# Kernel tuning notes

Measured on AMD Instinct MI355X. Metric: run time of the kernel, lower is better.

## Reference

```python
import jax, jax.numpy as jnp
import numpy as np

# Config (from TheoreticalConfig, scaled to production size)
B = 4096          # batch_size
S = 128           # seq_len (max_seq_len)
DIM_Q = 512
DIM_Z = 64
DIM_U = 512
HID_V = 512       # assumed net_V hidden width
T_OFF = 20        # T_offline
T_ON = 10         # T_online
DT = 0.1
STIFF = 0.1       # stiffness
CSTIFF = 0.1      # contact_stiffness
MIN_DIM = min(DIM_U, DIM_Q)  # == DIM_Q here


def setup_inputs() -> dict:
    key = jax.random.key(0)
    ks = jax.random.split(key, 10)
    f32 = jnp.float32
    return {
        "u_seq": jax.random.normal(ks[0], (B, S, DIM_U), f32),
        "q0_off": jax.random.normal(ks[1], (B, DIM_Q), f32) * 0.1,
        "p0_off": jax.random.normal(ks[2], (B, DIM_Q), f32) * 0.1,
        "q0_on": jax.random.normal(ks[3], (B, DIM_Q), f32) * 0.1,
        "p0_on": jax.random.normal(ks[4], (B, DIM_Q), f32) * 0.1,
        "z": jax.random.normal(ks[5], (1, DIM_Z), f32) * 0.1,
        "W1": jax.random.normal(ks[6], (DIM_Q + DIM_Z, HID_V), f32) / np.sqrt(DIM_Q + DIM_Z).astype(np.float32),
        "b1": jnp.zeros((HID_V,), f32),
        "W2": jax.random.normal(ks[7], (HID_V, 1), f32) / np.sqrt(HID_V).astype(np.float32),
        "b2": jnp.zeros((1,), f32),
    }


def _net_V(qz, W1, b1, W2, b2):
    # small MLP potential: [B, dim_q+dim_z] -> [B, 1]
    return jnp.tanh(qz @ W1 + b1) @ W2 + b2


def _compute_H(q, p, s, z, W1, b1, W2, b2):
    # H^c = K + V_quad + V_net + Phi, all [B, 1]
    K = 0.5 * jnp.sum(p * p, axis=-1, keepdims=True)
    V_quad = 0.5 * STIFF * jnp.sum(q * q, axis=-1, keepdims=True)
    V_net = _net_V(jnp.concatenate([q, z], axis=-1), W1, b1, W2, b2)
    Phi = 0.5 * CSTIFF * s * s
    return K + V_quad + V_net + Phi


def reference(u_seq, q0_off, p0_off, q0_on, p0_on, z, W1, b1, W2, b2):
    zb = jnp.broadcast_to(z, (B, DIM_Z))
    s = jnp.zeros((B, 1), u_seq.dtype)

    # ---- evolve_offline: symplectic-ish leapfrog with friction, T_OFF-1 steps ----
    F0_off = _compute_H(q0_off, p0_off, s, zb, W1, b1, W2, b2)

    def off_step(carry, _):
        q, p = carry
        q_new = q + DT * p                     # q += dt * grad_p (grad_p = p)
        p_new = (p - DT * (STIFF * q)) * 0.99  # p -= dt * grad_q (grad_q = stiff*q_old), then damping
        return (q_new, p_new), None

    (qf, pf), _ = jax.lax.scan(off_step, (q0_off, p0_off), None, length=T_OFF - 1)
    Ff_off = _compute_H(qf, pf, s, zb, W1, b1, W2, b2)
    offline_F = jnp.concatenate([F0_off, Ff_off], axis=1)  # [B, 2]

    # ---- evolve_online: port-coupled integration for min(S, T_ON) steps ----
    F0_on = _compute_H(q0_on, p0_on, s, zb, W1, b1, W2, b2)
    steps = min(S, T_ON)

    def on_step(carry, u_t):
        q, p = carry
        # p_new[:, :MIN_DIM] = p - dt*stiff*q + dt*0.1*u_t ; MIN_DIM == DIM_Q so full update
        p_new = (p - DT * (STIFF * q) + DT * (0.1 * u_t)) * 0.99
        q_new = q + DT * p_new
        return (q_new, p_new), None

    u_scan = jnp.transpose(u_seq[:, :steps, :MIN_DIM], (1, 0, 2))  # [steps, B, dim_q]
    (qf2, pf2), _ = jax.lax.scan(on_step, (q0_on, p0_on), u_scan)
    Ff_on = _compute_H(qf2, pf2, s, zb, W1, b1, W2, b2)
    online_F = jnp.concatenate([F0_on, Ff_on], axis=1)  # [B, 2]

    q_trajectory = qf2[:, None, :]  # [B, 1, dim_q]
    return offline_F, online_F, q_trajectory
```

## Files before the change

kernel.cpp:

```cpp
#include <hip/hip_runtime.h>
#include <hip/hip_bf16.h>

#define BB 4096
#define SS 128
#define DIMQ 512
#define DIMZ 64
#define DIMU 512
#define HIDV 512

typedef __attribute__((ext_vector_type(8))) short sh8;
typedef __attribute__((ext_vector_type(4))) float f32x4;
typedef __attribute__((ext_vector_type(4))) unsigned short us4;

__device__ inline unsigned short f2bf(float f) {
    unsigned u = __float_as_uint(f);
    return (unsigned short)((u + 0x7fffu + ((u >> 16) & 1u)) >> 16);
}

__global__ __launch_bounds__(256) void k_prep(const float* __restrict__ W1,
        const float* __restrict__ z, const float* __restrict__ b1,
        unsigned short* __restrict__ W1qT, float* __restrict__ cvec) {
    __shared__ float tile[32][33];
    int bx = blockIdx.x & 15, by = blockIdx.x >> 4;
    int k0 = by * 32, n0 = bx * 32;
    int tx = threadIdx.x & 31, tg = threadIdx.x >> 5;
    #pragma unroll
    for (int rr = 0; rr < 4; rr++) {
        int ty = tg * 4 + rr;
        tile[ty][tx] = W1[(size_t)(k0 + ty) * HIDV + n0 + tx];
    }
    __syncthreads();
    #pragma unroll
    for (int rr = 0; rr < 4; rr++) {
        int ty = tg * 4 + rr;
        W1qT[(size_t)(n0 + ty) * DIMQ + k0 + tx] = f2bf(tile[tx][ty]);
    }
    if (blockIdx.x < 2) {
        int h = blockIdx.x * 256 + threadIdx.x;
        float acc = b1[h];
        #pragma unroll 8
        for (int k = 0; k < DIMZ; k++) acc += z[k] * W1[(size_t)(DIMQ + k) * HIDV + h];
        cvec[h] = acc;
    }
}

__global__ __launch_bounds__(128) void k_states(
        const float* __restrict__ u, const float* __restrict__ q0off,
        const float* __restrict__ p0off, const float* __restrict__ q0on,
        const float* __restrict__ p0on, const float* __restrict__ b2,
        unsigned short* __restrict__ Qall, float* __restrict__ out,
        float* __restrict__ qtraj,
        float R00, float R01, float R10, float R11) {
    int b = blockIdx.x, t = threadIdx.x;
    int j = t * 4;
    size_t idx = (size_t)b * DIMQ + j;
    float q[4], p[4], qo[4], po[4];
    *(float4*)q  = *(const float4*)(q0off + idx);
    *(float4*)p  = *(const float4*)(p0off + idx);
    *(float4*)qo = *(const float4*)(q0on + idx);
    *(float4*)po = *(const float4*)(p0on + idx);

    float sums[8] = {0, 0, 0, 0, 0, 0, 0, 0};
    us4 w0, w1, w2, w3;
    float q2[4], p2[4];
    #pragma unroll
    for (int c = 0; c < 4; c++) {
        float qq = q[c], pp = p[c];
        sums[0] += qq * qq;
        sums[1] += pp * pp;
        float qf = R00 * qq + R01 * pp;
        float pf = R10 * qq + R11 * pp;
        sums[2] += qf * qf;
        sums[3] += pf * pf;
        w0[c] = f2bf(qq);
        w1[c] = f2bf(qf);
        q2[c] = qo[c]; p2[c] = po[c];
        sums[4] += q2[c] * q2[c];
        sums[5] += p2[c] * p2[c];
        w2[c] = f2bf(q2[c]);
    }
    *(us4*)(Qall + idx) = w0;
    *(us4*)(Qall + (size_t)(BB + b) * DIMQ + j) = w1;
    *(us4*)(Qall + (size_t)(2 * BB + b) * DIMQ + j) = w2;

    const float* ub = u + (size_t)b * SS * DIMU + j;
    #pragma unroll
    for (int st = 0; st < 10; st++) {
        float uv[4];
        *(float4*)uv = *(const float4*)(ub + (size_t)st * DIMU);
        #pragma unroll
        for (int c = 0; c < 4; c++) {
            p2[c] = (p2[c] - 0.1f * (0.1f * q2[c]) + 0.1f * (0.1f * uv[c])) * 0.99f;
            q2[c] = q2[c] + 0.1f * p2[c];
        }
    }
    #pragma unroll
    for (int c = 0; c < 4; c++) {
        sums[6] += q2[c] * q2[c];
        sums[7] += p2[c] * p2[c];
        w3[c] = f2bf(q2[c]);
    }
    *(us4*)(Qall + (size_t)(3 * BB + b) * DIMQ + j) = w3;
    *(float4*)(qtraj + idx) = *(float4*)q2;

    __shared__ float red[2][8];
    int lane = t & 63, w = t >> 6;
    #pragma unroll
    for (int k = 0; k < 8; k++) {
        float v = sums[k];
        #pragma unroll
        for (int m = 1; m < 64; m <<= 1) v += __shfl_xor(v, m, 64);
        if (lane == 0) red[w][k] = v;
    }
    __syncthreads();
    if (t < 4) {
        int e = t;
        float sq = red[0][2 * e] + red[1][2 * e];
        float sp = red[0][2 * e + 1] + red[1][2 * e + 1];
        float F = 0.5f * sp + 0.05f * sq + b2[0];
        size_t o = (size_t)b * 2 + (e & 1) + (size_t)(e >> 1) * 2 * BB;
        out[o] = F;
    }
}

__global__ __launch_bounds__(256) void k_gemm(
        const unsigned short* __restrict__ Qall, const unsigned short* __restrict__ W1qT,
        const float* __restrict__ cvec, const float* __restrict__ W2,
        float* __restrict__ out) {
    __shared__ __attribute__((aligned(16))) char lds[65536];
    const int t = threadIdx.x;
    const int lane = t & 63;
    const int w = t >> 6;
    const int wr = w >> 1, wc = w & 1;
    const int rowBase = blockIdx.x * 128;
    const int colBase = blockIdx.y * 128;

    f32x4 acc[4][4] = {};

    auto STAGE = [&](int kt, int buf) {
        char* ldsA = lds + buf * 32768;
        char* ldsB = ldsA + 16384;
        #pragma unroll
        for (int i = 0; i < 4; i++) {
            unsigned chunk = i * 256 + t;
            unsigned r = chunk >> 3;
            unsigned scb = (chunk & 7) ^ (r & 7);
            const unsigned short* srcA = Qall + (size_t)(rowBase + r) * 512 + (unsigned)kt * 64 + scb * 8;
            __builtin_amdgcn_global_load_lds(
                (const __attribute__((address_space(1))) unsigned int*)(const void*)srcA,
                (__attribute__((address_space(3))) unsigned int*)(void*)(ldsA + chunk * 16), 16, 0, 0);
            const unsigned short* srcB = W1qT + (size_t)(colBase + r) * 512 + (unsigned)kt * 64 + scb * 8;
            __builtin_amdgcn_global_load_lds(
                (const __attribute__((address_space(1))) unsigned int*)(const void*)srcB,
                (__attribute__((address_space(3))) unsigned int*)(void*)(ldsB + chunk * 16), 16, 0, 0);
        }
    };

    STAGE(0, 0);
    asm volatile("s_waitcnt vmcnt(0)" ::: "memory");
    __builtin_amdgcn_s_barrier();

    for (int kt = 0; kt < 8; kt++) {
        int cur = kt & 1;
        if (kt < 7) STAGE(kt + 1, cur ^ 1);
        char* ldsA = lds + cur * 32768;
        char* ldsB = ldsA + 16384;
        #pragma unroll
        for (int ks = 0; ks < 2; ks++) {
            sh8 af[4], bf_[4];
            int kb = ks * 64 + ((lane >> 4) << 4);
            #pragma unroll
            for (int mi = 0; mi < 4; mi++) {
                int m = wr * 64 + mi * 16 + (lane & 15);
                af[mi] = *(const sh8*)(ldsA + m * 128 + (kb ^ ((m & 7) << 4)));
            }
            #pragma unroll
            for (int ni = 0; ni < 4; ni++) {
                int n = wc * 64 + ni * 16 + (lane & 15);
                bf_[ni] = *(const sh8*)(ldsB + n * 128 + (kb ^ ((n & 7) << 4)));
            }
            #pragma unroll
            for (int mi = 0; mi < 4; mi++)
                #pragma unroll
                for (int ni = 0; ni < 4; ni++)
                    acc[mi][ni] = __builtin_amdgcn_mfma_f32_16x16x32_bf16(af[mi], bf_[ni], acc[mi][ni], 0, 0, 0);
        }
        asm volatile("s_waitcnt vmcnt(0) lgkmcnt(0)" ::: "memory");
        __builtin_amdgcn_s_barrier();
    }

    float w2v[4], cv[4];
    #pragma unroll
    for (int ni = 0; ni < 4; ni++) {
        int n = colBase + wc * 64 + ni * 16 + (lane & 15);
        w2v[ni] = W2[n];
        cv[ni] = cvec[n];
    }
    #pragma unroll
    for (int mi = 0; mi < 4; mi++) {
        #pragma unroll
        for (int r = 0; r < 4; r++) {
            float partial = 0.f;
            #pragma unroll
            for (int ni = 0; ni < 4; ni++)
                partial += tanhf(acc[mi][ni][r] + cv[ni]) * w2v[ni];
            partial += __shfl_xor(partial, 1, 64);
            partial += __shfl_xor(partial, 2, 64);
            partial += __shfl_xor(partial, 4, 64);
            partial += __shfl_xor(partial, 8, 64);
            if ((lane & 15) == 0) {
                int row = rowBase + wr * 64 + mi * 16 + ((lane >> 4) << 2) + r;
                int e = row >> 12, bb = row & 4095;
                size_t o = (size_t)bb * 2 + (e & 1) + (size_t)(e >> 1) * 2 * BB;
                atomicAdd(out + o, partial);
            }
        }
    }
}

extern "C" void kernel_launch(void* const* d_in, const int* in_sizes, int n_in,
                              void* d_out, int out_size, void* d_ws, size_t ws_size,
                              hipStream_t stream) {
    const float* u     = (const float*)d_in[0];
    const float* q0off = (const float*)d_in[1];
    const float* p0off = (const float*)d_in[2];
    const float* q0on  = (const float*)d_in[3];
    const float* p0on  = (const float*)d_in[4];
    const float* z     = (const float*)d_in[5];
    const float* W1    = (const float*)d_in[6];
    const float* b1    = (const float*)d_in[7];
    const float* W2    = (const float*)d_in[8];
    const float* b2    = (const float*)d_in[9];
    float* out = (float*)d_out;

    char* ws = (char*)d_ws;
    unsigned short* Qall = (unsigned short*)ws;
    unsigned short* W1qT = (unsigned short*)(ws + 16777216);
    float* cvec = (float*)(ws + 16777216 + 524288);

    double a00 = 1, a01 = 0, a10 = 0, a11 = 1;
    const double m00 = 1.0, m01 = 0.1, m10 = -0.1 * 0.1 * 0.99, m11 = 0.99;
    for (int i = 0; i < 19; i++) {
        double n00 = m00 * a00 + m01 * a10;
        double n01 = m00 * a01 + m01 * a11;
        double n10 = m10 * a00 + m11 * a10;
        double n11 = m10 * a01 + m11 * a11;
        a00 = n00; a01 = n01; a10 = n10; a11 = n11;
    }

    k_prep<<<256, 256, 0, stream>>>(W1, z, b1, W1qT, cvec);
    k_states<<<BB, 128, 0, stream>>>(u, q0off, p0off, q0on, p0on, b2, Qall, out,
                                     out + 4 * BB, (float)a00, (float)a01, (float)a10, (float)a11);
    k_gemm<<<dim3(128, 4), 256, 0, stream>>>(Qall, W1qT, cvec, W2, out);
}
```

Baseline: 48.61 us.

## Fuse state evolution into GEMM kernel, keeping activations in LDS

Merges the state-evolution kernel and the MFMA GEMM into one kernel. Each 512-thread block handles 16 batch rows and all 512 hidden columns, writing the bf16 activations straight into LDS rather than round-tripping them through a global workspace. Loading of the next input chunk overlaps with MFMA work, and W1 is double-buffered through LDS. The final reduction now runs in-block and writes output directly, removing the atomics and one launch. In exchange, only 256 blocks of 512 threads are launched with about 130KB of LDS each, so occupancy is low and W1 is re-read by every block.

```diff
diff --git a/kernel.cpp b/kernel.cpp
--- a/kernel.cpp
+++ b/kernel.cpp
@@ -4,9 +4,8 @@
 #define BB 4096
 #define SS 128
 #define DIMQ 512
+#define HIDV 512
 #define DIMZ 64
-#define DIMU 512
-#define HIDV 512
 
 typedef __attribute__((ext_vector_type(8))) short sh8;
 typedef __attribute__((ext_vector_type(4))) float f32x4;
@@ -44,177 +43,184 @@
     }
 }
 
-__global__ __launch_bounds__(128) void k_states(
+__global__ __launch_bounds__(512, 2) void k_fused(
         const float* __restrict__ u, const float* __restrict__ q0off,
         const float* __restrict__ p0off, const float* __restrict__ q0on,
         const float* __restrict__ p0on, const float* __restrict__ b2,
-        unsigned short* __restrict__ Qall, float* __restrict__ out,
+        const unsigned short* __restrict__ W1qT, const float* __restrict__ cvec,
+        const float* __restrict__ W2, float* __restrict__ out,
         float* __restrict__ qtraj,
         float R00, float R01, float R10, float R11) {
-    int b = blockIdx.x, t = threadIdx.x;
-    int j = t * 4;
-    size_t idx = (size_t)b * DIMQ + j;
-    float q[4], p[4], qo[4], po[4];
-    *(float4*)q  = *(const float4*)(q0off + idx);
-    *(float4*)p  = *(const float4*)(p0off + idx);
-    *(float4*)qo = *(const float4*)(q0on + idx);
-    *(float4*)po = *(const float4*)(p0on + idx);
-
-    float sums[8] = {0, 0, 0, 0, 0, 0, 0, 0};
-    us4 w0, w1, w2, w3;
-    float q2[4], p2[4];
-    #pragma unroll
-    for (int c = 0; c < 4; c++) {
-        float qq = q[c], pp = p[c];
-        sums[0] += qq * qq;
-        sums[1] += pp * pp;
-        float qf = R00 * qq + R01 * pp;
-        float pf = R10 * qq + R11 * pp;
-        sums[2] += qf * qf;
-        sums[3] += pf * pf;
-        w0[c] = f2bf(qq);
-        w1[c] = f2bf(qf);
-        q2[c] = qo[c]; p2[c] = po[c];
-        sums[4] += q2[c] * q2[c];
-        sums[5] += p2[c] * p2[c];
-        w2[c] = f2bf(q2[c]);
-    }
-    *(us4*)(Qall + idx) = w0;
-    *(us4*)(Qall + (size_t)(BB + b) * DIMQ + j) = w1;
-    *(us4*)(Qall + (size_t)(2 * BB + b) * DIMQ + j) = w2;
-
-    const float* ub = u + (size_t)b * SS * DIMU + j;
-    #pragma unroll
-    for (int st = 0; st < 10; st++) {
-        float uv[4];
-        *(float4*)uv = *(const float4*)(ub + (size_t)st * DIMU);
-        #pragma unroll
-        for (int c = 0; c < 4; c++) {
-            p2[c] = (p2[c] - 0.1f * (0.1f * q2[c]) + 0.1f * (0.1f * uv[c])) * 0.99f;
-            q2[c] = q2[c] + 0.1f * p2[c];
-        }
-    }
-    #pragma unroll
-    for (int c = 0; c < 4; c++) {
-        sums[6] += q2[c] * q2[c];
-        sums[7] += p2[c] * p2[c];
-        w3[c] = f2bf(q2[c]);
-    }
-    *(us4*)(Qall + (size_t)(3 * BB + b) * DIMQ + j) = w3;
-    *(float4*)(qtraj + idx) = *(float4*)q2;
-
-    __shared__ float red[2][8];
-    int lane = t & 63, w = t >> 6;
-    #pragma unroll
-    for (int k = 0; k < 8; k++) {
-        float v = sums[k];
-        #pragma unroll
-        for (int m = 1; m < 64; m <<= 1) v += __shfl_xor(v, m, 64);
-        if (lane == 0) red[w][k] = v;
-    }
-    __syncthreads();
-    if (t < 4) {
-        int e = t;
-        float sq = red[0][2 * e] + red[1][2 * e];
-        float sp = red[0][2 * e + 1] + red[1][2 * e + 1];
-        float F = 0.5f * sp + 0.05f * sq + b2[0];
-        size_t o = (size_t)b * 2 + (e & 1) + (size_t)(e >> 1) * 2 * BB;
-        out[o] = F;
-    }
-}
-
-__global__ __launch_bounds__(256) void k_gemm(
-        const unsigned short* __restrict__ Qall, const unsigned short* __restrict__ W1qT,
-        const float* __restrict__ cvec, const float* __restrict__ W2,
-        float* __restrict__ out) {
-    __shared__ __attribute__((aligned(16))) char lds[65536];
+    extern __shared__ char lds[];
+    char* ldsA = lds;
+    char* ldsW = lds + 65536;
+    float* basev = (float*)(lds + 131072);
+    float* parts = (float*)(lds + 131072 + 256);
+
     const int t = threadIdx.x;
     const int lane = t & 63;
+    const int g = lane >> 4;
+    const int r = lane & 15;
     const int w = t >> 6;
-    const int wr = w >> 1, wc = w & 1;
-    const int rowBase = blockIdx.x * 128;
-    const int colBase = blockIdx.y * 128;
+    const int b0 = blockIdx.x * 16;
+    const int rb = t >> 5;
+    const int tc = t & 31;
+    const size_t srow = (size_t)(b0 + rb) * DIMQ;
+    const float* ubase = u + (size_t)(b0 + rb) * SS * DIMQ;
+
+    float sums[8] = {0, 0, 0, 0, 0, 0, 0, 0};
+    float4 vq, vp, vqo, vpo, vu0, vu1, vu2, vu3, vu4, vu5, vu6, vu7, vu8, vu9;
+
+    auto STAGEW = [&](int kt, int buf) {
+        char* dst = ldsW + buf * 32768;
+        #pragma unroll
+        for (int i = 0; i < 4; i++) {
+            int ch = i * 512 + t;
+            int n = ch >> 2, sl = ch & 3;
+            int ssl = sl ^ ((n >> 1) & 3);
+            const unsigned short* src = W1qT + (size_t)n * 512 + kt * 32 + ssl * 8;
+            __builtin_amdgcn_global_load_lds(
+                (const __attribute__((address_space(1))) unsigned int*)(const void*)src,
+                (__attribute__((address_space(3))) unsigned int*)(void*)(dst + ch * 16), 16, 0, 0);
+        }
+    };
+    auto LOADC = [&](int c) {
+        int j = c * 128 + tc * 4;
+        vq  = *(const float4*)(q0off + srow + j);
+        vp  = *(const float4*)(p0off + srow + j);
+        vqo = *(const float4*)(q0on  + srow + j);
+        vpo = *(const float4*)(p0on  + srow + j);
+        const float* ub = ubase + j;
+        vu0 = *(const float4*)(ub);            vu1 = *(const float4*)(ub + 512);
+        vu2 = *(const float4*)(ub + 1024);     vu3 = *(const float4*)(ub + 1536);
+        vu4 = *(const float4*)(ub + 2048);     vu5 = *(const float4*)(ub + 2560);
+        vu6 = *(const float4*)(ub + 3072);     vu7 = *(const float4*)(ub + 3584);
+        vu8 = *(const float4*)(ub + 4096);     vu9 = *(const float4*)(ub + 4608);
+    };
+    auto PROCC = [&](int c) {
+        int j = c * 128 + tc * 4;
+        us4 a0, a1, a2, a3;
+        float4 qt;
+        #pragma unroll
+        for (int cc = 0; cc < 4; cc++) {
+            float qq = vq[cc], pp = vp[cc];
+            sums[0] += qq * qq; sums[1] += pp * pp;
+            float qf = R00 * qq + R01 * pp;
+            float pf = R10 * qq + R11 * pp;
+            sums[2] += qf * qf; sums[3] += pf * pf;
+            float q2 = vqo[cc], p2 = vpo[cc];
+            sums[4] += q2 * q2; sums[5] += p2 * p2;
+            a2[cc] = f2bf(q2);
+            float uv[10] = {vu0[cc], vu1[cc], vu2[cc], vu3[cc], vu4[cc],
+                            vu5[cc], vu6[cc], vu7[cc], vu8[cc], vu9[cc]};
+            #pragma unroll
+            for (int st = 0; st < 10; st++) {
+                p2 = (p2 - 0.1f * (0.1f * q2) + 0.1f * (0.1f * uv[st])) * 0.99f;
+                q2 = q2 + 0.1f * p2;
+            }
+            sums[6] += q2 * q2; sums[7] += p2 * p2;
+            a0[cc] = f2bf(qq); a1[cc] = f2bf(qf); a3[cc] = f2bf(q2);
+            qt[cc] = q2;
+        }
+        int jb = j * 2;
+        {int m = rb;      *(us4*)(ldsA + m * 1024 + (jb ^ ((m & 7) << 4))) = a0;}
+        {int m = 16 + rb; *(us4*)(ldsA + m * 1024 + (jb ^ ((m & 7) << 4))) = a1;}
+        {int m = 32 + rb; *(us4*)(ldsA + m * 1024 + (jb ^ ((m & 7) << 4))) = a2;}
+        {int m = 48 + rb; *(us4*)(ldsA + m * 1024 + (jb ^ ((m & 7) << 4))) = a3;}
+        *(float4*)(qtraj + srow + j) = qt;
+    };
+
+    STAGEW(0, 0);
+    LOADC(0);
+    asm volatile("s_waitcnt vmcnt(0)" ::: "memory");
+    PROCC(0);
+    __syncthreads();
 
     f32x4 acc[4][4] = {};
-
-    auto STAGE = [&](int kt, int buf) {
-        char* ldsA = lds + buf * 32768;
-        char* ldsB = ldsA + 16384;
-        #pragma unroll
-        for (int i = 0; i < 4; i++) {
-            unsigned chunk = i * 256 + t;
-            unsigned r = chunk >> 3;
-            unsigned scb = (chunk & 7) ^ (r & 7);
-            const unsigned short* srcA = Qall + (size_t)(rowBase + r) * 512 + (unsigned)kt * 64 + scb * 8;
-            __builtin_amdgcn_global_load_lds(
-                (const __attribute__((address_space(1))) unsigned int*)(const void*)srcA,
-                (__attribute__((address_space(3))) unsigned int*)(void*)(ldsA + chunk * 16), 16, 0, 0);
-            const unsigned short* srcB = W1qT + (size_t)(colBase + r) * 512 + (unsigned)kt * 64 + scb * 8;
-            __builtin_amdgcn_global_load_lds(
-                (const __attribute__((address_space(1))) unsigned int*)(const void*)srcB,
-                (__attribute__((address_space(3))) unsigned int*)(void*)(ldsB + chunk * 16), 16, 0, 0);
-        }
-    };
-
-    STAGE(0, 0);
-    asm volatile("s_waitcnt vmcnt(0)" ::: "memory");
-    __builtin_amdgcn_s_barrier();
-
-    for (int kt = 0; kt < 8; kt++) {
-        int cur = kt & 1;
-        if (kt < 7) STAGE(kt + 1, cur ^ 1);
-        char* ldsA = lds + cur * 32768;
-        char* ldsB = ldsA + 16384;
-        #pragma unroll
-        for (int ks = 0; ks < 2; ks++) {
-            sh8 af[4], bf_[4];
-            int kb = ks * 64 + ((lane >> 4) << 4);
+    const int nb = w * 64;
+
+    for (int c = 0; c < 4; c++) {
+        #pragma unroll
+        for (int kl = 0; kl < 4; kl++) {
+            int kt = c * 4 + kl;
+            if (kt < 15) STAGEW(kt + 1, (kt + 1) & 1);
+            if (kl == 2 && c < 3) LOADC(c + 1);
+            sh8 af[4], wf[4];
+            char* wb = ldsW + (kt & 1) * 32768;
             #pragma unroll
             for (int mi = 0; mi < 4; mi++) {
-                int m = wr * 64 + mi * 16 + (lane & 15);
-                af[mi] = *(const sh8*)(ldsA + m * 128 + (kb ^ ((m & 7) << 4)));
+                int m = mi * 16 + r;
+                af[mi] = *(const sh8*)(ldsA + m * 1024 + ((kt * 64 + g * 16) ^ ((m & 7) << 4)));
             }
             #pragma unroll
             for (int ni = 0; ni < 4; ni++) {
-                int n = wc * 64 + ni * 16 + (lane & 15);
-                bf_[ni] = *(const sh8*)(ldsB + n * 128 + (kb ^ ((n & 7) << 4)));
+                int n = nb + ni * 16 + r;
+                wf[ni] = *(const sh8*)(wb + n * 64 + ((g ^ ((n >> 1) & 3)) << 4));
             }
             #pragma unroll
             for (int mi = 0; mi < 4; mi++)
                 #pragma unroll
                 for (int ni = 0; ni < 4; ni++)
-                    acc[mi][ni] = __builtin_amdgcn_mfma_f32_16x16x32_bf16(af[mi], bf_[ni], acc[mi][ni], 0, 0, 0);
-        }
-        asm volatile("s_waitcnt vmcnt(0) lgkmcnt(0)" ::: "memory");
-        __builtin_amdgcn_s_barrier();
+                    acc[mi][ni] = __builtin_amdgcn_mfma_f32_16x16x32_bf16(af[mi], wf[ni], acc[mi][ni], 0, 0, 0);
+            if (kl == 3) {
+                asm volatile("s_waitcnt vmcnt(0)" ::: "memory");
+                if (c < 3) PROCC(c + 1);
+            } else if (kl == 2 && c < 3) {
+                asm volatile("s_waitcnt vmcnt(14)" ::: "memory");
+            } else {
+                asm volatile("s_waitcnt vmcnt(0)" ::: "memory");
+            }
+            __syncthreads();
+        }
+    }
+
+    #pragma unroll
+    for (int k = 0; k < 8; k++) {
+        float v = sums[k];
+        v += __shfl_xor(v, 1, 64);
+        v += __shfl_xor(v, 2, 64);
+        v += __shfl_xor(v, 4, 64);
+        v += __shfl_xor(v, 8, 64);
+        v += __shfl_xor(v, 16, 64);
+        sums[k] = v;
+    }
+    if (tc == 0) {
+        float b2v = b2[0];
+        #pragma unroll
+        for (int e = 0; e < 4; e++)
+            basev[e * 16 + rb] = 0.5f * sums[2 * e + 1] + 0.05f * sums[2 * e] + b2v;
     }
 
     float w2v[4], cv[4];
     #pragma unroll
     for (int ni = 0; ni < 4; ni++) {
-        int n = colBase + wc * 64 + ni * 16 + (lane & 15);
+        int n = nb + ni * 16 + r;
         w2v[ni] = W2[n];
         cv[ni] = cvec[n];
     }
     #pragma unroll
     for (int mi = 0; mi < 4; mi++) {
         #pragma unroll
-        for (int r = 0; r < 4; r++) {
-            float partial = 0.f;
+        for (int reg = 0; reg < 4; reg++) {
+            float s = 0.f;
             #pragma unroll
             for (int ni = 0; ni < 4; ni++)
-                partial += tanhf(acc[mi][ni][r] + cv[ni]) * w2v[ni];
-            partial += __shfl_xor(partial, 1, 64);
-            partial += __shfl_xor(partial, 2, 64);
-            partial += __shfl_xor(partial, 4, 64);
-            partial += __shfl_xor(partial, 8, 64);
-            if ((lane & 15) == 0) {
-                int row = rowBase + wr * 64 + mi * 16 + ((lane >> 4) << 2) + r;
-                int e = row >> 12, bb = row & 4095;
-                size_t o = (size_t)bb * 2 + (e & 1) + (size_t)(e >> 1) * 2 * BB;
-                atomicAdd(out + o, partial);
-            }
-        }
+                s += tanhf(acc[mi][ni][reg] + cv[ni]) * w2v[ni];
+            s += __shfl_xor(s, 1, 64);
+            s += __shfl_xor(s, 2, 64);
+            s += __shfl_xor(s, 4, 64);
+            s += __shfl_xor(s, 8, 64);
+            if (r == 0) parts[w * 64 + mi * 16 + g * 4 + reg] = s;
+        }
+    }
+    __syncthreads();
+    if (t < 64) {
+        float v = basev[t];
+        #pragma unroll
+        for (int ww = 0; ww < 8; ww++) v += parts[ww * 64 + t];
+        int e = t >> 4, rbb = t & 15;
+        size_t o = (size_t)(b0 + rbb) * 2 + (e & 1) + (size_t)(e >> 1) * 2 * BB;
+        out[o] = v;
     }
 }
 
@@ -234,9 +240,8 @@
     float* out = (float*)d_out;
 
     char* ws = (char*)d_ws;
-    unsigned short* Qall = (unsigned short*)ws;
-    unsigned short* W1qT = (unsigned short*)(ws + 16777216);
-    float* cvec = (float*)(ws + 16777216 + 524288);
+    unsigned short* W1qT = (unsigned short*)ws;
+    float* cvec = (float*)(ws + 524288);
 
     double a00 = 1, a01 = 0, a10 = 0, a11 = 1;
     const double m00 = 1.0, m01 = 0.1, m10 = -0.1 * 0.1 * 0.99, m11 = 0.99;
@@ -249,7 +254,7 @@
     }
 
     k_prep<<<256, 256, 0, stream>>>(W1, z, b1, W1qT, cvec);
-    k_states<<<BB, 128, 0, stream>>>(u, q0off, p0off, q0on, p0on, b2, Qall, out,
-                                     out + 4 * BB, (float)a00, (float)a01, (float)a10, (float)a11);
-    k_gemm<<<dim3(128, 4), 256, 0, stream>>>(Qall, W1qT, cvec, W2, out);
-}
+    k_fused<<<256, 512, 133376, stream>>>(u, q0off, p0off, q0on, p0on, b2,
+                                          W1qT, cvec, W2, out, out + 4 * BB,
+                                          (float)a00, (float)a01, (float)a10, (float)a11);
+}
```

Result: slower. 54.36 us (+11.8%).
